# Kernel optimization log

Hardware: AMD Instinct MI355X
Metric: run time of the kernel (lower is better)

## Reference

```python
import jax, jax.numpy as jnp
import numpy as np

LEN = 2048

def setup_inputs() -> dict:
    key = jax.random.key(0)
    k1, k2 = jax.random.split(key)
    x = jax.random.normal(k1, (LEN,), dtype=jnp.float32)
    y = jax.random.normal(k2, (LEN,), dtype=jnp.float32)
    return {"x": x, "y": y}

def reference(x, y):
    # Classic DTW DP with squared-difference cost.
    # Original torch code clamps indices with max(i-1,0)/max(j-1,0); because
    # DTW[i,j] is still +inf when read, the clamped reads reduce to the
    # standard recurrence: row 0 is a cumulative sum, col 0 uses only 'up',
    # interior uses min(up, left, diag).
    inf = jnp.float32(jnp.inf)
    cost0 = (x[0] - y) ** 2            # [len2]
    row0 = jnp.cumsum(cost0)           # DTW row i=0

    def row_step(prev_row, xi):
        cost = (xi - y) ** 2                                   # [len2]
        diag = jnp.concatenate([prev_row[:1], prev_row[:-1]])  # prev_row[j-1], clamped at j=0
        def cell(left, cud):
            c, up, dg = cud
            v = c + jnp.minimum(jnp.minimum(up, left), dg)
            return v, v
        # left init = inf => at j=0 min reduces to min(up, diag) = prev_row[0]
        _, new_row = jax.lax.scan(cell, inf, (cost, prev_row, diag))
        return new_row, None

    last_row, _ = jax.lax.scan(row_step, row0, x[1:])
    return jnp.sqrt(last_row[-1])
```

## Files before the change

kernel.cpp:

```cpp
#include <hip/hip_runtime.h>
#include <math.h>


#define NLEN  2048
#define NW    4
#define CSTEP 64
#define DSKEW 128
#define PAD   64
#define RROW  (PAD + 2112)
#define GTOT  2496
#define INFV  1e30f

__device__ __forceinline__ float dpp_shr1(float v, float inj) {
    int r = __builtin_amdgcn_update_dpp(
        __builtin_bit_cast(int, inj), __builtin_bit_cast(int, v),
        0x138 , 0xF, 0xF, false );
    return __builtin_bit_cast(float, r);
}
__device__ __forceinline__ float rdlane(float v, int l) {
    return __builtin_bit_cast(float,
        __builtin_amdgcn_readlane(__builtin_bit_cast(int, v), l));
}
__device__ __forceinline__ float min3f(float a, float b, float c) {
    unsigned ia = __builtin_bit_cast(unsigned, a);
    unsigned ib = __builtin_bit_cast(unsigned, b);
    unsigned ic = __builtin_bit_cast(unsigned, c);
    unsigned m  = __builtin_elementwise_min(
                      __builtin_elementwise_min(ia, ib), ic);
    return __builtin_bit_cast(float, m);
}

__global__ __launch_bounds__(256, 1) void dtw_kernel(const float* __restrict__ X,
                                                     const float* __restrict__ Y,
                                                     float* __restrict__ out) {
    __shared__ __align__(16) float yS[NLEN];
    __shared__ float ring[(NW + 1) * RROW];

    const int tid  = threadIdx.x;
    const int w    = tid >> 6;
    const int lane = tid & 63;

    {
        const float4* Y4 = (const float4*)Y;
        float4* y4 = (float4*)yS;
        y4[tid]       = Y4[tid];
        y4[tid + 256] = Y4[tid + 256];
    }
    for (int k = tid; k < (NW + 1) * RROW; k += 256) ring[k] = INFV;
    __syncthreads();

    float x0, x1, x2, x3, x4, x5, x6, x7;
    {
        const float4 xa = *(const float4*)&X[tid * 8];
        const float4 xb = *(const float4*)&X[tid * 8 + 4];
        x0 = xa.x; x1 = xa.y; x2 = xa.z; x3 = xa.w;
        x4 = xb.x; x5 = xb.y; x6 = xb.z; x7 = xb.w;
    }

    float v0 = INFV, v1 = INFV, v2 = INFV, v3 = INFV;
    float v4 = INFV, v5 = INFV, v6 = INFV, v7 = INFV;
    float uprev = (tid == 0) ? 0.0f : INFV;
    float yconv = 0.0f;

    const float* ringR = ring + w * RROW + PAD;
    float*       ringW = ring + (w + 1) * RROW + PAD;

    for (int gb = 0; gb < GTOT; gb += CSTEP) {
        const int tau0 = gb - w * DSKEW;

        if (tau0 >= 0 && tau0 <= NLEN) {
            int yi = tau0 + lane;
            if (yi >= NLEN) yi = NLEN - 1;
            const float yblk = yS[yi];
            const float rblk = ringR[tau0 + lane];
            float* wp = ringW + (tau0 - lane);
            const bool isout = (tau0 == NLEN) & (w == NW - 1) & (lane == 63);

            #pragma unroll
            for (int s = 0; s < CSTEP; ++s) {
                const float yu = rdlane(yblk, s);
                const float ru = rdlane(rblk, s);
                yconv = dpp_shr1(yconv, yu);
                const float u = dpp_shr1(v7, ru);
                float d0 = x0 - yconv; float nv0 = fmaf(d0, d0, min3f(v0, uprev, u));
                float d1 = x1 - yconv; float nv1 = fmaf(d1, d1, min3f(v1, v0, nv0));
                float d2 = x2 - yconv; float nv2 = fmaf(d2, d2, min3f(v2, v1, nv1));
                float d3 = x3 - yconv; float nv3 = fmaf(d3, d3, min3f(v3, v2, nv2));
                float d4 = x4 - yconv; float nv4 = fmaf(d4, d4, min3f(v4, v3, nv3));
                float d5 = x5 - yconv; float nv5 = fmaf(d5, d5, min3f(v5, v4, nv4));
                float d6 = x6 - yconv; float nv6 = fmaf(d6, d6, min3f(v6, v5, nv5));
                float d7 = x7 - yconv; float nv7 = fmaf(d7, d7, min3f(v7, v6, nv6));
                wp[s] = nv7;
                uprev = u;
                v0 = nv0; v1 = nv1; v2 = nv2; v3 = nv3;
                v4 = nv4; v5 = nv5; v6 = nv6; v7 = nv7;
                if (s == 62 && isout) out[0] = sqrtf(nv7);
            }
        }
        __syncthreads();
    }
}

extern "C" void kernel_launch(void* const* d_in, const int* in_sizes, int n_in,
                              void* d_out, int out_size, void* d_ws, size_t ws_size,
                              hipStream_t stream) {
    const float* x = (const float*)d_in[0];
    const float* y = (const float*)d_in[1];
    (void)in_sizes; (void)n_in; (void)out_size; (void)d_ws; (void)ws_size;
    dtw_kernel<<<1, 256, 0, stream>>>(x, y, (float*)d_out);
}
```

Before: 198.2 us.

## Skew rows within each thread so per-step cell updates become independent

Each thread's eight rows now run on a wavefront skewed by one column per row, so all eight cell updates in a step depend only on the previous step's values. This breaks the serial min/fma chain across rows and exposes instruction-level parallelism. The inter-wave ring buffer is rearranged into an 8-way strided layout with a larger skew and padding to match the new write pattern. In exchange the pipeline gets longer (more total steps and warp skew), register use rises from the extra delay registers, and the indexing is more intricate.

Result: slower. 297.4 us (+50.0%).

```diff
diff --git a/kernel.cpp b/kernel.cpp
--- a/kernel.cpp
+++ b/kernel.cpp
@@ -2,14 +2,16 @@
 #include <math.h>
 
 
-#define NLEN  2048
-#define NW    4
-#define CSTEP 64
-#define DSKEW 128
-#define PAD   64
-#define RROW  (PAD + 2112)
-#define GTOT  2496
-#define INFV  1e30f
+#define NLEN   2048
+#define NW     4
+#define CSTEP  64
+#define DSKEW  576
+#define PAD    512
+#define RSTR   386
+#define RROW   (8 * RSTR)
+#define TAUMAX 2496
+#define GTOT   (TAUMAX + CSTEP + (NW - 1) * DSKEW)
+#define INFV   1e30f
 
 __device__ __forceinline__ float dpp_shr1(float v, float inj) {
     int r = __builtin_amdgcn_update_dpp(
@@ -57,44 +59,50 @@
         x4 = xb.x; x5 = xb.y; x6 = xb.z; x7 = xb.w;
     }
 
-    float v0 = INFV, v1 = INFV, v2 = INFV, v3 = INFV;
-    float v4 = INFV, v5 = INFV, v6 = INFV, v7 = INFV;
+    float c0 = INFV, c1 = INFV, c2 = INFV, c3 = INFV;
+    float c4 = INFV, c5 = INFV, c6 = INFV, c7 = INFV;
+    float o0 = INFV, o1 = INFV, o2 = INFV, o3 = INFV;
+    float o4 = INFV, o5 = INFV, o6 = INFV;
+    float y0 = 0.0f, y1 = 0.0f, y2 = 0.0f, y3 = 0.0f;
+    float y4r = 0.0f, y5 = 0.0f, y6 = 0.0f, y7 = 0.0f;
     float uprev = (tid == 0) ? 0.0f : INFV;
-    float yconv = 0.0f;
 
-    const float* ringR = ring + w * RROW + PAD;
-    float*       ringW = ring + (w + 1) * RROW + PAD;
+    const float* ringR = ring + w * RROW;
+    float*       ringW = ring + (w + 1) * RROW;
 
     for (int gb = 0; gb < GTOT; gb += CSTEP) {
         const int tau0 = gb - w * DSKEW;
 
-        if (tau0 >= 0 && tau0 <= NLEN) {
+        if (tau0 >= 0 && tau0 <= TAUMAX) {
             int yi = tau0 + lane;
             if (yi >= NLEN) yi = NLEN - 1;
             const float yblk = yS[yi];
-            const float rblk = ringR[tau0 + lane];
-            float* wp = ringW + (tau0 - lane);
-            const bool isout = (tau0 == NLEN) & (w == NW - 1) & (lane == 63);
+            const float rblk = ringR[(lane & 7) * RSTR + (tau0 >> 3) + 64 + (lane >> 3)];
+            float* wbase = ringW + (tau0 >> 3) - lane;
+            const bool isout = (tau0 == TAUMAX) & (w == NW - 1) & (lane == 63);
 
             #pragma unroll
             for (int s = 0; s < CSTEP; ++s) {
                 const float yu = rdlane(yblk, s);
                 const float ru = rdlane(rblk, s);
-                yconv = dpp_shr1(yconv, yu);
-                const float u = dpp_shr1(v7, ru);
-                float d0 = x0 - yconv; float nv0 = fmaf(d0, d0, min3f(v0, uprev, u));
-                float d1 = x1 - yconv; float nv1 = fmaf(d1, d1, min3f(v1, v0, nv0));
-                float d2 = x2 - yconv; float nv2 = fmaf(d2, d2, min3f(v2, v1, nv1));
-                float d3 = x3 - yconv; float nv3 = fmaf(d3, d3, min3f(v3, v2, nv2));
-                float d4 = x4 - yconv; float nv4 = fmaf(d4, d4, min3f(v4, v3, nv3));
-                float d5 = x5 - yconv; float nv5 = fmaf(d5, d5, min3f(v5, v4, nv4));
-                float d6 = x6 - yconv; float nv6 = fmaf(d6, d6, min3f(v6, v5, nv5));
-                float d7 = x7 - yconv; float nv7 = fmaf(d7, d7, min3f(v7, v6, nv6));
-                wp[s] = nv7;
+                const float yn = dpp_shr1(y7, yu);
+                const float u  = dpp_shr1(c7, ru);
+                float d0 = x0 - yn;  float n0 = fmaf(d0, d0, min3f(c0, u,  uprev));
+                float d1 = x1 - y0;  float n1 = fmaf(d1, d1, min3f(c1, c0, o0));
+                float d2 = x2 - y1;  float n2 = fmaf(d2, d2, min3f(c2, c1, o1));
+                float d3 = x3 - y2;  float n3 = fmaf(d3, d3, min3f(c3, c2, o2));
+                float d4 = x4 - y3;  float n4 = fmaf(d4, d4, min3f(c4, c3, o3));
+                float d5 = x5 - y4r; float n5 = fmaf(d5, d5, min3f(c5, c4, o4));
+                float d6 = x6 - y5;  float n6 = fmaf(d6, d6, min3f(c6, c5, o5));
+                float d7 = x7 - y6;  float n7 = fmaf(d7, d7, min3f(c7, c6, o6));
+                wbase[((s + 1) & 7) * RSTR + ((s + 505) >> 3)] = n7;
                 uprev = u;
-                v0 = nv0; v1 = nv1; v2 = nv2; v3 = nv3;
-                v4 = nv4; v5 = nv5; v6 = nv6; v7 = nv7;
-                if (s == 62 && isout) out[0] = sqrtf(nv7);
+                o0 = c0; o1 = c1; o2 = c2; o3 = c3; o4 = c4; o5 = c5; o6 = c6;
+                c0 = n0; c1 = n1; c2 = n2; c3 = n3;
+                c4 = n4; c5 = n5; c6 = n6; c7 = n7;
+                y7 = y6; y6 = y5; y5 = y4r; y4r = y3;
+                y3 = y2; y2 = y1; y1 = y0; y0 = yn;
+                if (s == 62 && isout) out[0] = sqrtf(n7);
             }
         }
         __syncthreads();
```

## Process two anti-diagonal columns per step with per-lane y vector loads

Applied to the files above, without the earlier changes.

Restructures the wavefront so each lane handles two consecutive y positions per inner step, halving the number of cross-lane DPP shifts per column. Each lane now loads its own skewed y values straight from padded shared memory as float2 instead of broadcasting them with readlane and shifting them through DPP. The x-minus-y differences use packed two-wide float vectors, and the ring writes become 8-byte stores. The skew, padding and tau bounds change to fit the doubled diagonal width. The price is more registers held per lane and more LDS reads.

Result: faster. 181.2 us (-8.6%).

```diff
diff --git a/kernel.cpp b/kernel.cpp
--- a/kernel.cpp
+++ b/kernel.cpp
@@ -2,14 +2,19 @@
 #include <math.h>
 
 
-#define NLEN  2048
-#define NW    4
-#define CSTEP 64
-#define DSKEW 128
-#define PAD   64
-#define RROW  (PAD + 2112)
-#define GTOT  2496
-#define INFV  1e30f
+#define NLEN   2048
+#define NW     4
+#define CSTEP  64
+#define SPB    (CSTEP / 2)
+#define DSKEW  192
+#define PAD    128
+#define RROW   (PAD + 2176)
+#define YPAD   128
+#define TAUMAX 2112
+#define GTOT   (TAUMAX + (NW - 1) * DSKEW + CSTEP)
+#define INFV   1e30f
+
+typedef float f32x2 __attribute__((ext_vector_type(2)));
 
 __device__ __forceinline__ float dpp_shr1(float v, float inj) {
     int r = __builtin_amdgcn_update_dpp(
@@ -33,8 +38,9 @@
 __global__ __launch_bounds__(256, 1) void dtw_kernel(const float* __restrict__ X,
                                                      const float* __restrict__ Y,
                                                      float* __restrict__ out) {
-    __shared__ __align__(16) float yS[NLEN];
+    __shared__ __align__(16) float yB[YPAD + NLEN + YPAD];
     __shared__ float ring[(NW + 1) * RROW];
+    float* yS = yB + YPAD;
 
     const int tid  = threadIdx.x;
     const int w    = tid >> 6;
@@ -42,25 +48,31 @@
 
     {
         const float4* Y4 = (const float4*)Y;
-        float4* y4 = (float4*)yS;
+        float4* y4 = (float4*)(yB + YPAD);
         y4[tid]       = Y4[tid];
         y4[tid + 256] = Y4[tid + 256];
+        if (tid < YPAD) {
+            yB[tid]               = INFV;
+            yB[YPAD + NLEN + tid] = INFV;
+        }
     }
     for (int k = tid; k < (NW + 1) * RROW; k += 256) ring[k] = INFV;
     __syncthreads();
 
-    float x0, x1, x2, x3, x4, x5, x6, x7;
+    f32x2 xx0, xx1, xx2, xx3, xx4, xx5, xx6, xx7;
     {
         const float4 xa = *(const float4*)&X[tid * 8];
         const float4 xb = *(const float4*)&X[tid * 8 + 4];
-        x0 = xa.x; x1 = xa.y; x2 = xa.z; x3 = xa.w;
-        x4 = xb.x; x5 = xb.y; x6 = xb.z; x7 = xb.w;
+        xx0 = (f32x2){xa.x, xa.x}; xx1 = (f32x2){xa.y, xa.y};
+        xx2 = (f32x2){xa.z, xa.z}; xx3 = (f32x2){xa.w, xa.w};
+        xx4 = (f32x2){xb.x, xb.x}; xx5 = (f32x2){xb.y, xb.y};
+        xx6 = (f32x2){xb.z, xb.z}; xx7 = (f32x2){xb.w, xb.w};
     }
 
-    float v0 = INFV, v1 = INFV, v2 = INFV, v3 = INFV;
-    float v4 = INFV, v5 = INFV, v6 = INFV, v7 = INFV;
-    float uprev = (tid == 0) ? 0.0f : INFV;
-    float yconv = 0.0f;
+    float pB0 = INFV, pB1 = INFV, pB2 = INFV, pB3 = INFV;
+    float pB4 = INFV, pB5 = INFV, pB6 = INFV, pB7 = INFV;
+    float a7p = INFV;
+    float uBp = (tid == 0) ? 0.0f : INFV;
 
     const float* ringR = ring + w * RROW + PAD;
     float*       ringW = ring + (w + 1) * RROW + PAD;
@@ -68,33 +80,54 @@
     for (int gb = 0; gb < GTOT; gb += CSTEP) {
         const int tau0 = gb - w * DSKEW;
 
-        if (tau0 >= 0 && tau0 <= NLEN) {
-            int yi = tau0 + lane;
-            if (yi >= NLEN) yi = NLEN - 1;
-            const float yblk = yS[yi];
+        if (tau0 >= 0 && tau0 <= TAUMAX) {
             const float rblk = ringR[tau0 + lane];
-            float* wp = ringW + (tau0 - lane);
-            const bool isout = (tau0 == NLEN) & (w == NW - 1) & (lane == 63);
+            f32x2 y2[SPB];
+            {
+                const f32x2* yp = (const f32x2*)(yS + (tau0 - 2 * lane));
+                #pragma unroll
+                for (int k = 0; k < SPB; ++k) y2[k] = yp[k];
+            }
+            float* wp = ringW + (tau0 - 2 * lane);
+            const bool isout = (tau0 == TAUMAX) & (w == NW - 1) & (lane == 63);
 
             #pragma unroll
-            for (int s = 0; s < CSTEP; ++s) {
-                const float yu = rdlane(yblk, s);
-                const float ru = rdlane(rblk, s);
-                yconv = dpp_shr1(yconv, yu);
-                const float u = dpp_shr1(v7, ru);
-                float d0 = x0 - yconv; float nv0 = fmaf(d0, d0, min3f(v0, uprev, u));
-                float d1 = x1 - yconv; float nv1 = fmaf(d1, d1, min3f(v1, v0, nv0));
-                float d2 = x2 - yconv; float nv2 = fmaf(d2, d2, min3f(v2, v1, nv1));
-                float d3 = x3 - yconv; float nv3 = fmaf(d3, d3, min3f(v3, v2, nv2));
-                float d4 = x4 - yconv; float nv4 = fmaf(d4, d4, min3f(v4, v3, nv3));
-                float d5 = x5 - yconv; float nv5 = fmaf(d5, d5, min3f(v5, v4, nv4));
-                float d6 = x6 - yconv; float nv6 = fmaf(d6, d6, min3f(v6, v5, nv5));
-                float d7 = x7 - yconv; float nv7 = fmaf(d7, d7, min3f(v7, v6, nv6));
-                wp[s] = nv7;
-                uprev = u;
-                v0 = nv0; v1 = nv1; v2 = nv2; v3 = nv3;
-                v4 = nv4; v5 = nv5; v6 = nv6; v7 = nv7;
-                if (s == 62 && isout) out[0] = sqrtf(nv7);
+            for (int s = 0; s < SPB; ++s) {
+                const float riA = rdlane(rblk, 2 * s);
+                const float riB = rdlane(rblk, 2 * s + 1);
+                const float uA  = dpp_shr1(a7p, riA);
+                const float uB  = dpp_shr1(pB7, riB);
+                const f32x2 yv = y2[s];
+                f32x2 d0 = xx0 - yv;
+                float n0A = fmaf(d0.x, d0.x, min3f(pB0, uA,  uBp));
+                float n0B = fmaf(d0.y, d0.y, min3f(n0A, uB,  uA));
+                f32x2 d1 = xx1 - yv;
+                float n1A = fmaf(d1.x, d1.x, min3f(pB1, n0A, pB0));
+                float n1B = fmaf(d1.y, d1.y, min3f(n1A, n0B, n0A));
+                f32x2 d2 = xx2 - yv;
+                float n2A = fmaf(d2.x, d2.x, min3f(pB2, n1A, pB1));
+                float n2B = fmaf(d2.y, d2.y, min3f(n2A, n1B, n1A));
+                f32x2 d3 = xx3 - yv;
+                float n3A = fmaf(d3.x, d3.x, min3f(pB3, n2A, pB2));
+                float n3B = fmaf(d3.y, d3.y, min3f(n3A, n2B, n2A));
+                f32x2 d4 = xx4 - yv;
+                float n4A = fmaf(d4.x, d4.x, min3f(pB4, n3A, pB3));
+                float n4B = fmaf(d4.y, d4.y, min3f(n4A, n3B, n3A));
+                f32x2 d5 = xx5 - yv;
+                float n5A = fmaf(d5.x, d5.x, min3f(pB5, n4A, pB4));
+                float n5B = fmaf(d5.y, d5.y, min3f(n5A, n4B, n4A));
+                f32x2 d6 = xx6 - yv;
+                float n6A = fmaf(d6.x, d6.x, min3f(pB6, n5A, pB5));
+                float n6B = fmaf(d6.y, d6.y, min3f(n6A, n5B, n5A));
+                f32x2 d7 = xx7 - yv;
+                float n7A = fmaf(d7.x, d7.x, min3f(pB7, n6A, pB6));
+                float n7B = fmaf(d7.y, d7.y, min3f(n7A, n6B, n6A));
+                f32x2 wv; wv.x = n7A; wv.y = n7B;
+                *(f32x2*)(wp + 2 * s) = wv;
+                uBp = uB; a7p = n7A;
+                pB0 = n0B; pB1 = n1B; pB2 = n2B; pB3 = n3B;
+                pB4 = n4B; pB5 = n5B; pB6 = n6B; pB7 = n7B;
+                if (s == 30 && isout) out[0] = sqrtf(n7B);
             }
         }
         __syncthreads();
```
